# Kernel optimization log

Measured on AMD Instinct MI355X. Metric: run time of the kernel, lower is better.

The kernel has to match this reference:

```python
import jax, jax.numpy as jnp
import numpy as np

B = 4096          # walker batch
S0, S1 = 8, 8     # up / down spins
N = S0 + S1       # total electrons
M = 4             # nucleons
D = 16            # determinants
N_ONE = [256, 256, 256, 256]
N_TWO = [32, 32, 32, 32]


def setup_inputs() -> dict:
    key = jax.random.key(0)
    ks = jax.random.split(key, 16)
    f0 = 8 + 3 * 4 * M              # 56, first-layer one-stream input
    f1 = 3 * N_ONE[0] + 2 * N_TWO[0]  # 832, later-layer one-stream input
    s = 0.05
    return {
        "x": jax.random.normal(ks[0], (B, N, 3), jnp.float32),
        "nucleon_pos": jnp.asarray([[0.0, 0.0, 0.0], [0.0, 0.0, 1.4],
                                    [1.2, 0.0, 0.0], [0.0, 1.2, 0.7]], jnp.float32),
        "v0_w": s * jax.random.normal(ks[1], (N_ONE[0], f0), jnp.float32),
        "v0_b": s * jax.random.normal(ks[2], (N_ONE[0],), jnp.float32),
        "v_w": s * jax.random.normal(ks[3], (3, N_ONE[0], f1), jnp.float32),
        "v_b": s * jax.random.normal(ks[4], (3, N_ONE[0]), jnp.float32),
        "w0_w": s * jax.random.normal(ks[5], (N_TWO[0], 4), jnp.float32),
        "w0_b": s * jax.random.normal(ks[6], (N_TWO[0],), jnp.float32),
        "w_w": s * jax.random.normal(ks[7], (3, N_TWO[0], N_TWO[0]), jnp.float32),
        "w_b": s * jax.random.normal(ks[8], (3, N_TWO[0]), jnp.float32),
        "env_w": s * jax.random.normal(ks[9], (D, N, N_ONE[-1]), jnp.float32),
        "env_g": jax.random.uniform(ks[10], (D, N), jnp.float32),
        "sigma": jax.random.uniform(ks[11], (D, N, M), jnp.float32),
        "pi": jax.random.uniform(ks[12], (D, N, M), jnp.float32),
    }


def _safe_norm(v, axis):
    # ||v||_2 with a zero (not NaN) gradient at v == 0 (diagonal e-e distances).
    s = jnp.sum(v * v, axis=axis)
    return jnp.sqrt(jnp.where(s == 0, 1.0, s)) * (s > 0)


def reference(x, nucleon_pos, v0_w, v0_b, v_w, v_b, w0_w, w0_b, w_w, w_b,
              env_w, env_g, sigma, pi):
    b = x.shape[0]
    # electron-electron stream: [B,N,N,4], [b,i,j] = x_j - x_i, |x_j - x_i|
    tev = x[:, None, :, :] - x[:, :, None, :]
    two = jnp.concatenate([tev, _safe_norm(tev, -1)[..., None]], axis=-1)
    # electron-nucleus: oev[b,m,n] = x_n - R_m  -> [B,M,N,3]
    oev = x[:, None, :, :] - nucleon_pos[:, None, :]
    oed = jnp.linalg.norm(oev, axis=-1)                     # [B,M,N]
    one = jnp.concatenate([oev, oed[..., None]], axis=-1)   # [B,M,N,4]
    one = jnp.transpose(one, (0, 2, 1, 3)).reshape(b, N, 4 * M)  # [B,N,4M]
    oev_p = jnp.transpose(oev, (0, 2, 1, 3))                # [B,N,M,3]

    for l in range(len(N_ONE)):
        g1u = jnp.mean(one[:, :S0], axis=1)                 # [B,F]
        g1d = jnp.mean(one[:, S0:], axis=1)
        g2u = jnp.mean(two[:, :, :S0, :], axis=2)           # [B,N,F2]
        g2d = jnp.mean(two[:, :, S0:, :], axis=2)
        f = jnp.concatenate([
            one,
            jnp.broadcast_to(g1u[:, None], (b, N, g1u.shape[-1])),
            jnp.broadcast_to(g1d[:, None], (b, N, g1d.shape[-1])),
            g2u, g2d], axis=-1)
        Wv, bv = (v0_w, v0_b) if l == 0 else (v_w[l - 1], v_b[l - 1])
        Ww, bw = (w0_w, w0_b) if l == 0 else (w_w[l - 1], w_b[l - 1])
        new_one = jnp.tanh(jnp.einsum('bnf,of->bno', f, Wv) + bv)
        new_two = jnp.tanh(jnp.einsum('bijf,of->bijo', two, Ww) + bw)
        if l > 0 and N_ONE[l] == N_ONE[l - 1] and N_TWO[l] == N_TWO[l - 1]:
            new_one = new_one + one
            new_two = new_two + two
        one, two = new_one, new_two

    r = jnp.linalg.norm(oev_p, axis=-1)                     # [B,N,M]
    F = N_ONE[-1]

    def block(rows, cols):
        ew = env_w[:, rows]                # [D,ni,F]
        eg = env_g[:, rows]                # [D,ni]
        sg = jnp.abs(sigma[:, rows])       # [D,ni,M]
        pw = pi[:, rows]                   # [D,ni,M]
        h = one[:, cols]                   # [B,nj,F]
        rj = r[:, cols]                    # [B,nj,M]
        # sum_f (w*h + g) = w.h + F*g
        lin = jnp.einsum('kif,bjf->bkij', ew, h) + F * eg[None, :, :, None]
        env = jnp.zeros(lin.shape, lin.dtype)
        for m in range(M):                 # small static loop over nucleons
            env = env + pw[None, :, :, None, m] * jnp.exp(
                -sg[None, :, :, None, m] * rj[:, None, None, :, m])
        return lin * env                   # [B,D,ni,nj]

    psi_up = block(slice(0, S0), slice(0, S0))
    psi_dn = block(slice(0, S1), slice(S0, N))  # original reuses row params k*N+i
    d = jnp.linalg.det(psi_up) * jnp.linalg.det(psi_dn)     # [B,D]
    return jnp.sum(d, axis=1)                               # [B]
```

## Files before the change

### kernel.cpp

```cpp
#include <hip/hip_runtime.h>
#include <cmath>

namespace {

typedef unsigned short u16;
typedef unsigned int u32;
using short8  = __attribute__((ext_vector_type(8))) short;
using float4v = __attribute__((ext_vector_type(4))) float;

constexpr size_t MB_HI  = 0;
constexpr size_t MB_LO  = 638976;
constexpr size_t L0_HI  = 1277952;
constexpr size_t L0_LO  = L0_HI + 16384;
constexpr size_t ENV_HI = L0_LO + 16384;
constexpr size_t ENV_LO = ENV_HI + 32768;

__device__ __forceinline__ u16 f2bf(float f) {
    u32 u = __float_as_uint(f);
    u += 0x7FFFu + ((u >> 16) & 1u);
    return (u16)(u >> 16);
}
__device__ __forceinline__ float bf2f(u16 h) {
    return __uint_as_float(((u32)h) << 16);
}
__device__ __forceinline__ float fast_tanh(float x) {
    float e = __expf(-2.f * fabsf(x));
    float t = (1.f - e) * __builtin_amdgcn_rcpf(1.f + e);
    return copysignf(t, x);
}

__global__ void k_prep_main(const float* __restrict__ vw, u16* __restrict__ hi, u16* __restrict__ lo) {
    int id = blockIdx.x * 256 + threadIdx.x;
    int l = id / 212992, rem = id % 212992;
    int ks = rem >> 13;
    int r2 = rem & 8191;
    int nt = r2 >> 9, lane = (r2 >> 3) & 63, j = r2 & 7;
    int n = nt * 16 + (lane & 15);
    int f = ks * 32 + ((lane >> 4) << 3) + j;
    float w = vw[(size_t)(l * 256 + n) * 832 + f];
    u16 h = f2bf(w);
    hi[id] = h; lo[id] = f2bf(w - bf2f(h));
}
__global__ void k_prep_l0(const float* __restrict__ v0w, u16* __restrict__ hi, u16* __restrict__ lo) {
    int id = blockIdx.x * 256 + threadIdx.x;
    int ks = id >> 13;
    int r2 = id & 8191;
    int nt = r2 >> 9, lane = (r2 >> 3) & 63, j = r2 & 7;
    int n = nt * 16 + (lane & 15);
    int f = ks * 32 + ((lane >> 4) << 3) + j;
    float w = (f < 56) ? v0w[n * 56 + f] : 0.f;
    u16 h = f2bf(w);
    hi[id] = h; lo[id] = f2bf(w - bf2f(h));
}
__global__ void k_prep_env(const float* __restrict__ ew, u16* __restrict__ hi, u16* __restrict__ lo) {
    int id = blockIdx.x * 256 + threadIdx.x;
    int ks = id >> 12;
    int r2 = id & 4095;
    int nt = r2 >> 9, lane = (r2 >> 3) & 63, j = r2 & 7;
    int n = nt * 16 + (lane & 15);
    int f = ks * 32 + ((lane >> 4) << 3) + j;
    float w = ew[(size_t)(((n >> 3) * 16) + (n & 7)) * 256 + f];
    u16 h = f2bf(w);
    hi[id] = h; lo[id] = f2bf(w - bf2f(h));
}

template <bool L0, bool RES, bool LAST>
__device__ __forceinline__ void layer_run(
    int t, float (&two)[32], float (&prev)[4][4],
    u16 (*stateF)[32][16][8], u16 (*g2F)[8][16][8], float (*g1s)[256],
    const u16* __restrict__ Bhi, const u16* __restrict__ Blo,
    const float* __restrict__ bvp,
    const float* __restrict__ wwp, const float* __restrict__ bwp)
{
    const int lane = t & 63, wv = t >> 6, quad = lane >> 4, l16 = lane & 15;
    float4v acc[4];
    #pragma unroll
    for (int q = 0; q < 4; ++q) acc[q] = (float4v){0.f, 0.f, 0.f, 0.f};

    const size_t wb0 = (size_t)(wv * 4) * 512 + (size_t)lane * 8;

    auto mfma_step = [&](int ks, short8 Ah, short8 Al) {
        const u16* bh = Bhi + wb0 + (size_t)ks * 8192;
        const u16* bl = Blo + wb0 + (size_t)ks * 8192;
        #pragma unroll
        for (int q = 0; q < 4; ++q) {
            short8 Wh = *(const short8*)(bh + q * 512);
            short8 Wl = *(const short8*)(bl + q * 512);
            acc[q] = __builtin_amdgcn_mfma_f32_16x16x32_bf16(Ah, Wh, acc[q], 0, 0, 0);
            acc[q] = __builtin_amdgcn_mfma_f32_16x16x32_bf16(Al, Wh, acc[q], 0, 0, 0);
            acc[q] = __builtin_amdgcn_mfma_f32_16x16x32_bf16(Ah, Wl, acc[q], 0, 0, 0);
        }
    };

    if (L0) {
        #pragma unroll
        for (int ks = 0; ks < 2; ++ks) {
            short8 Ah = *(const short8*)&g2F[0][ks * 4 + quad][l16][0];
            short8 Al = *(const short8*)&g2F[1][ks * 4 + quad][l16][0];
            mfma_step(ks, Ah, Al);
        }
    } else {
        #pragma unroll 2
        for (int ks = 0; ks < 8; ++ks) {
            short8 Ah = *(const short8*)&stateF[0][ks * 4 + quad][l16][0];
            short8 Al = *(const short8*)&stateF[1][ks * 4 + quad][l16][0];
            mfma_step(ks, Ah, Al);
        }
        #pragma unroll 2
        for (int ks = 8; ks < 24; ++ks) {
            const int ud = (ks < 16) ? 0 : 1;
            const int c0 = ((ks - 8) & 7) * 32 + quad * 8;
            const float* gp = &g1s[ud][c0];
            short8 Ah, Al;
            #pragma unroll
            for (int j = 0; j < 8; ++j) {
                float f = gp[j];
                u16 h = f2bf(f);
                Ah[j] = (short)h;
                Al[j] = (short)f2bf(f - bf2f(h));
            }
            mfma_step(ks, Ah, Al);
        }
        #pragma unroll
        for (int ks = 24; ks < 26; ++ks) {
            short8 Ah = *(const short8*)&g2F[0][(ks - 24) * 4 + quad][l16][0];
            short8 Al = *(const short8*)&g2F[1][(ks - 24) * 4 + quad][l16][0];
            mfma_step(ks, Ah, Al);
        }
    }
    __syncthreads();

    #pragma unroll
    for (int q = 0; q < 4; ++q) {
        const int n = (wv * 4 + q) * 16 + l16;
        const float bvv = bvp[n];
        #pragma unroll
        for (int r = 0; r < 4; ++r) {
            float v = fast_tanh(acc[q][r] + bvv);
            if (RES) v += prev[q][r];
            prev[q][r] = v;
        }
        if (!LAST) {
            float su = 0.f, sd = 0.f;
            #pragma unroll
            for (int r = 0; r < 4; ++r) { if (quad < 2) su += prev[q][r]; else sd += prev[q][r]; }
            su += __shfl_xor(su, 16); su += __shfl_xor(su, 32);
            sd += __shfl_xor(sd, 16); sd += __shfl_xor(sd, 32);
            if (quad == 0) { g1s[0][n] = su * 0.125f; g1s[1][n] = sd * 0.125f; }
        }
        const int ko = n >> 3, jj = n & 7;
        #pragma unroll
        for (int r = 0; r < 4; ++r) {
            const int m = quad * 4 + r;
            u16 h = f2bf(prev[q][r]);
            stateF[0][ko][m][jj] = h;
            stateF[1][ko][m][jj] = f2bf(prev[q][r] - bf2f(h));
        }
    }

    if (!LAST) {
        constexpr int TIN = L0 ? 4 : 32;
        float nt2[32];
        #pragma unroll 4
        for (int o = 0; o < 32; ++o) {
            float a = bwp[o];
            #pragma unroll
            for (int c = 0; c < TIN; ++c) a += two[c] * wwp[o * TIN + c];
            nt2[o] = fast_tanh(a);
            if (RES) nt2[o] += two[o];
        }
        #pragma unroll
        for (int o = 0; o < 32; ++o) two[o] = nt2[o];
        const int i = t >> 4, ud = (t >> 3) & 1;
        #pragma unroll
        for (int c = 0; c < 32; ++c) {
            float v = two[c];
            v += __shfl_xor(v, 1); v += __shfl_xor(v, 2); v += __shfl_xor(v, 4);
            if ((t & 7) == 0) {
                float mn = v * 0.125f;
                int k = ud * 32 + c;
                u16 h = f2bf(mn);
                g2F[0][k >> 3][i][k & 7] = h;
                g2F[1][k >> 3][i][k & 7] = f2bf(mn - bf2f(h));
            }
        }
    }
    __syncthreads();
}

__global__ __launch_bounds__(256, 4) void ferminet_kernel(
    const float* __restrict__ x,
    const float* __restrict__ nuc,
    const float* __restrict__ v0_b,
    const float* __restrict__ v_b,
    const float* __restrict__ w0_w,
    const float* __restrict__ w0_b,
    const float* __restrict__ w_w,
    const float* __restrict__ w_b,
    const float* __restrict__ env_g,
    const float* __restrict__ sigma,
    const float* __restrict__ pi_,
    const u16* __restrict__ wsB,
    float* __restrict__ out)
{
    __shared__ u16  stateF[2][32][16][8];
    __shared__ u16  g2F[2][8][16][8];
    __shared__ float g1s[2][256];
    __shared__ float xs[48];
    __shared__ float rs[64];
    __shared__ float dets[2][16];
    float* psi = (float*)&stateF[0][0][0][0];

    const int t = threadIdx.x;
    const int b = blockIdx.x;
    const int lane = t & 63, wv = t >> 6, quad = lane >> 4, l16 = lane & 15;

    if (t < 48) xs[t] = x[(size_t)b * 48 + t];
    if (t >= 128 && t < 192) ((u32*)&g2F[0][7][0][0])[t - 128] = 0u;
    if (t >= 192 && t < 256) ((u32*)&g2F[1][7][0][0])[t - 192] = 0u;
    __syncthreads();

    if (t < 64) {
        int n = t >> 2, m = t & 3;
        float ox = xs[n * 3 + 0] - nuc[m * 3 + 0];
        float oy = xs[n * 3 + 1] - nuc[m * 3 + 1];
        float oz = xs[n * 3 + 2] - nuc[m * 3 + 2];
        float d = sqrtf(ox * ox + oy * oy + oz * oz);
        rs[n * 4 + m] = d;
        float v[4] = {ox, oy, oz, d};
        #pragma unroll
        for (int c = 0; c < 4; ++c) {
            int k = m * 4 + c;
            u16 h = f2bf(v[c]);
            g2F[0][k >> 3][n][k & 7] = h;
            g2F[1][k >> 3][n][k & 7] = f2bf(v[c] - bf2f(h));
        }
        #pragma unroll
        for (int c = 0; c < 4; ++c) {
            float s = v[c];
            s += __shfl_xor(s, 4); s += __shfl_xor(s, 8); s += __shfl_xor(s, 16);
            if ((n & 7) == 0) {
                float mn = s * 0.125f;
                int k = 16 + (n >> 3) * 16 + m * 4 + c;
                u16 h = f2bf(mn);
                u16 lo = f2bf(mn - bf2f(h));
                #pragma unroll
                for (int mm = 0; mm < 16; ++mm) {
                    g2F[0][k >> 3][mm][k & 7] = h;
                    g2F[1][k >> 3][mm][k & 7] = lo;
                }
            }
        }
    }
    float two[32];
    {
        int i = t >> 4, j = t & 15;
        float dx = xs[j * 3 + 0] - xs[i * 3 + 0];
        float dy = xs[j * 3 + 1] - xs[i * 3 + 1];
        float dz = xs[j * 3 + 2] - xs[i * 3 + 2];
        float s2 = dx * dx + dy * dy + dz * dz;
        float nr = (s2 > 0.f) ? sqrtf(s2) : 0.f;
        two[0] = dx; two[1] = dy; two[2] = dz; two[3] = nr;
        #pragma unroll
        for (int c = 0; c < 4; ++c) {
            float v = two[c];
            v += __shfl_xor(v, 1); v += __shfl_xor(v, 2); v += __shfl_xor(v, 4);
            if ((t & 7) == 0) {
                float mn = v * 0.125f;
                int k = 48 + ((t >> 3) & 1) * 4 + c;
                u16 h = f2bf(mn);
                g2F[0][k >> 3][i][k & 7] = h;
                g2F[1][k >> 3][i][k & 7] = f2bf(mn - bf2f(h));
            }
        }
    }
    __syncthreads();

    float prev[4][4];
    layer_run<true,  false, false>(t, two, prev, stateF, g2F, g1s,
        wsB + L0_HI, wsB + L0_LO, v0_b, w0_w, w0_b);
    layer_run<false, true,  false>(t, two, prev, stateF, g2F, g1s,
        wsB + MB_HI + 0 * 212992, wsB + MB_LO + 0 * 212992, v_b + 0 * 256, w_w + 0 * 1024, w_b + 0 * 32);
    layer_run<false, true,  false>(t, two, prev, stateF, g2F, g1s,
        wsB + MB_HI + 1 * 212992, wsB + MB_LO + 1 * 212992, v_b + 1 * 256, w_w + 1 * 1024, w_b + 1 * 32);
    layer_run<false, true,  true >(t, two, prev, stateF, g2F, g1s,
        wsB + MB_HI + 2 * 212992, wsB + MB_LO + 2 * 212992, v_b + 2 * 256, w_w + 2 * 1024, w_b + 2 * 32);

    {
        float4v ac2[2];
        ac2[0] = (float4v){0.f, 0.f, 0.f, 0.f};
        ac2[1] = (float4v){0.f, 0.f, 0.f, 0.f};
        const size_t wb0 = (size_t)(wv * 2) * 512 + (size_t)lane * 8;
        const u16* Eh = wsB + ENV_HI;
        const u16* El = wsB + ENV_LO;
        #pragma unroll 2
        for (int ks = 0; ks < 8; ++ks) {
            short8 Ah = *(const short8*)&stateF[0][ks * 4 + quad][l16][0];
            short8 Al = *(const short8*)&stateF[1][ks * 4 + quad][l16][0];
            const u16* bh = Eh + wb0 + (size_t)ks * 4096;
            const u16* bl = El + wb0 + (size_t)ks * 4096;
            #pragma unroll
            for (int q = 0; q < 2; ++q) {
                short8 Wh = *(const short8*)(bh + q * 512);
                short8 Wl = *(const short8*)(bl + q * 512);
                ac2[q] = __builtin_amdgcn_mfma_f32_16x16x32_bf16(Ah, Wh, ac2[q], 0, 0, 0);
                ac2[q] = __builtin_amdgcn_mfma_f32_16x16x32_bf16(Al, Wh, ac2[q], 0, 0, 0);
                ac2[q] = __builtin_amdgcn_mfma_f32_16x16x32_bf16(Ah, Wl, ac2[q], 0, 0, 0);
            }
        }
        float vals[2][4];
        int kk[2], ii[2];
        #pragma unroll
        for (int q = 0; q < 2; ++q) {
            const int n = (wv * 2 + q) * 16 + l16;
            const int k = n >> 3, i = n & 7, kif = k * 16 + i;
            kk[q] = k; ii[q] = i;
            const float lc = 256.f * env_g[kif];
            const float4 pw4 = *(const float4*)&pi_[(size_t)kif * 4];
            const float4 sg4 = *(const float4*)&sigma[(size_t)kif * 4];
            const float sg[4] = {fabsf(sg4.x), fabsf(sg4.y), fabsf(sg4.z), fabsf(sg4.w)};
            const float pw[4] = {pw4.x, pw4.y, pw4.z, pw4.w};
            #pragma unroll
            for (int r = 0; r < 4; ++r) {
                const int je = quad * 4 + r;
                float E = 0.f;
                #pragma unroll
                for (int m = 0; m < 4; ++m) E += pw[m] * __expf(-sg[m] * rs[je * 4 + m]);
                vals[q][r] = (ac2[q][r] + lc) * E;
            }
        }
        __syncthreads();
        #pragma unroll
        for (int q = 0; q < 2; ++q) {
            #pragma unroll
            for (int r = 0; r < 4; ++r) {
                const int je = quad * 4 + r;
                const int s = je >> 3, j = je & 7;
                psi[((s * 16 + kk[q]) * 8 + ii[q]) * 8 + j] = vals[q][r];
            }
        }
    }
    __syncthreads();

    if (t < 32) {
        int s = t >> 4, k = t & 15;
        const float* src = psi + (s * 16 + k) * 64;
        float m[8][8];
        #pragma unroll
        for (int i = 0; i < 8; ++i)
            #pragma unroll
            for (int j = 0; j < 8; ++j) m[i][j] = src[i * 8 + j];
        float det = 1.f;
        #pragma unroll
        for (int c = 0; c < 8; ++c) {
            #pragma unroll
            for (int r = c + 1; r < 8; ++r) {
                if (fabsf(m[r][c]) > fabsf(m[c][c])) {
                    det = -det;
                    #pragma unroll
                    for (int j = 0; j < 8; ++j) {
                        float tmp = m[c][j]; m[c][j] = m[r][j]; m[r][j] = tmp;
                    }
                }
            }
            float piv = m[c][c];
            det *= piv;
            if (piv != 0.f) {
                float inv = 1.f / piv;
                #pragma unroll
                for (int r = c + 1; r < 8; ++r) {
                    float fac = m[r][c] * inv;
                    #pragma unroll
                    for (int j = c; j < 8; ++j) m[r][j] -= fac * m[c][j];
                }
            }
        }
        dets[s][k] = det;
    }
    __syncthreads();

    if (t == 0) {
        float s = 0.f;
        #pragma unroll
        for (int k = 0; k < 16; ++k) s += dets[0][k] * dets[1][k];
        out[b] = s;
    }
}

}

extern "C" void kernel_launch(void* const* d_in, const int* in_sizes, int n_in,
                              void* d_out, int out_size, void* d_ws, size_t ws_size,
                              hipStream_t stream) {
    (void)n_in; (void)out_size; (void)ws_size;
    const float* x    = (const float*)d_in[0];
    const float* nuc  = (const float*)d_in[1];
    const float* v0w  = (const float*)d_in[2];
    const float* v0b  = (const float*)d_in[3];
    const float* vw   = (const float*)d_in[4];
    const float* vb   = (const float*)d_in[5];
    const float* w0w  = (const float*)d_in[6];
    const float* w0b  = (const float*)d_in[7];
    const float* ww   = (const float*)d_in[8];
    const float* wb   = (const float*)d_in[9];
    const float* envw = (const float*)d_in[10];
    const float* envg = (const float*)d_in[11];
    const float* sig  = (const float*)d_in[12];
    const float* pii  = (const float*)d_in[13];
    float* out = (float*)d_out;
    u16* wsB = (u16*)d_ws;

    k_prep_main<<<638976 / 256, 256, 0, stream>>>(vw, wsB + MB_HI, wsB + MB_LO);
    k_prep_l0  <<<16384 / 256, 256, 0, stream>>>(v0w, wsB + L0_HI, wsB + L0_LO);
    k_prep_env <<<32768 / 256, 256, 0, stream>>>(envw, wsB + ENV_HI, wsB + ENV_LO);

    const int B = in_sizes[0] / 48;
    ferminet_kernel<<<B, 256, 0, stream>>>(x, nuc, v0b, vb, w0w, w0b,
                                           ww, wb, envg, sig, pii, wsB, out);
}
```

Before: 602.6 us.

## Move two-electron stream layers onto MFMA with split-bf16 weights in shared memory

Replaces the per-thread scalar FMA loop for the two-electron stream (32x32 per pair, per layer) with bf16 hi/lo split MFMA tiles. The two-stream state now lives in shared memory in fragment layout instead of registers, and its weights are preprocessed by a new prep kernel. The one-stream mean g1 is stored pre-split as bf16 fragments, so the MFMA loop no longer converts it from fp32 each step. Launch bounds drop from 4 to 2 waves per SIMD and LDS use grows, which may cut occupancy, and residuals are now rebuilt from bf16 hi+lo pairs.

```diff
diff --git a/kernel.cpp b/kernel.cpp
--- a/kernel.cpp
+++ b/kernel.cpp
@@ -8,12 +8,14 @@
 using short8  = __attribute__((ext_vector_type(8))) short;
 using float4v = __attribute__((ext_vector_type(4))) float;
 
-constexpr size_t MB_HI  = 0;
-constexpr size_t MB_LO  = 638976;
-constexpr size_t L0_HI  = 1277952;
-constexpr size_t L0_LO  = L0_HI + 16384;
-constexpr size_t ENV_HI = L0_LO + 16384;
-constexpr size_t ENV_LO = ENV_HI + 32768;
+constexpr size_t MB_HI   = 0;
+constexpr size_t MB_LO   = 638976;
+constexpr size_t L0_HI   = 1277952;
+constexpr size_t L0_LO   = L0_HI + 16384;
+constexpr size_t ENV_HI  = L0_LO + 16384;
+constexpr size_t ENV_LO  = ENV_HI + 32768;
+constexpr size_t TWOB_HI = ENV_LO + 32768;
+constexpr size_t TWOB_LO = TWOB_HI + 4096;
 
 __device__ __forceinline__ u16 f2bf(float f) {
     u32 u = __float_as_uint(f);
@@ -63,14 +65,28 @@
     u16 h = f2bf(w);
     hi[id] = h; lo[id] = f2bf(w - bf2f(h));
 }
+__global__ void k_prep_two(const float* __restrict__ w0w, const float* __restrict__ ww,
+                           u16* __restrict__ hi, u16* __restrict__ lo) {
+    int id = blockIdx.x * 256 + threadIdx.x;
+    int l = id >> 10, r = id & 1023;
+    int nt = r >> 9, lane = (r >> 3) & 63, j = r & 7;
+    int n = nt * 16 + (lane & 15);
+    int f = ((lane >> 4) << 3) + j;
+    float w;
+    if (l == 0) w = (f < 4) ? w0w[n * 4 + f] : 0.f;
+    else        w = ww[(size_t)(((l - 1) * 32) + n) * 32 + f];
+    u16 h = f2bf(w);
+    hi[id] = h; lo[id] = f2bf(w - bf2f(h));
+}
 
 template <bool L0, bool RES, bool LAST>
 __device__ __forceinline__ void layer_run(
-    int t, float (&two)[32], float (&prev)[4][4],
-    u16 (*stateF)[32][16][8], u16 (*g2F)[8][16][8], float (*g1s)[256],
+    int t, float (&prev)[4][4],
+    u16 (*stateF)[32][16][8], u16 (*twoF)[16][4][16][8],
+    u16 (*g2F)[8][16][8], u16 (*g1F)[2][8][4][8],
     const u16* __restrict__ Bhi, const u16* __restrict__ Blo,
-    const float* __restrict__ bvp,
-    const float* __restrict__ wwp, const float* __restrict__ bwp)
+    const u16* __restrict__ TBhi, const u16* __restrict__ TBlo,
+    const float* __restrict__ bvp, const float* __restrict__ bwp)
 {
     const int lane = t & 63, wv = t >> 6, quad = lane >> 4, l16 = lane & 15;
     float4v acc[4];
@@ -106,19 +122,12 @@
             short8 Al = *(const short8*)&stateF[1][ks * 4 + quad][l16][0];
             mfma_step(ks, Ah, Al);
         }
-        #pragma unroll 2
+        #pragma unroll 4
         for (int ks = 8; ks < 24; ++ks) {
             const int ud = (ks < 16) ? 0 : 1;
-            const int c0 = ((ks - 8) & 7) * 32 + quad * 8;
-            const float* gp = &g1s[ud][c0];
-            short8 Ah, Al;
-            #pragma unroll
-            for (int j = 0; j < 8; ++j) {
-                float f = gp[j];
-                u16 h = f2bf(f);
-                Ah[j] = (short)h;
-                Al[j] = (short)f2bf(f - bf2f(h));
-            }
+            const int kg = (ks - 8) & 7;
+            short8 Ah = *(const short8*)&g1F[0][ud][kg][quad][0];
+            short8 Al = *(const short8*)&g1F[1][ud][kg][quad][0];
             mfma_step(ks, Ah, Al);
         }
         #pragma unroll
@@ -128,6 +137,32 @@
             mfma_step(ks, Ah, Al);
         }
     }
+
+    float4v tac[4][2];
+    #pragma unroll
+    for (int mt = 0; mt < 4; ++mt)
+        #pragma unroll
+        for (int nt = 0; nt < 2; ++nt) tac[mt][nt] = (float4v){0.f, 0.f, 0.f, 0.f};
+    {
+        short8 TWh[2], TWl[2];
+        #pragma unroll
+        for (int nt = 0; nt < 2; ++nt) {
+            TWh[nt] = *(const short8*)(TBhi + nt * 512 + (size_t)lane * 8);
+            TWl[nt] = *(const short8*)(TBlo + nt * 512 + (size_t)lane * 8);
+        }
+        #pragma unroll
+        for (int mt = 0; mt < 4; ++mt) {
+            const int it = wv * 4 + mt;
+            short8 Ah = *(const short8*)&twoF[0][it][quad][l16][0];
+            short8 Al = *(const short8*)&twoF[1][it][quad][l16][0];
+            #pragma unroll
+            for (int nt = 0; nt < 2; ++nt) {
+                tac[mt][nt] = __builtin_amdgcn_mfma_f32_16x16x32_bf16(Ah, TWh[nt], tac[mt][nt], 0, 0, 0);
+                tac[mt][nt] = __builtin_amdgcn_mfma_f32_16x16x32_bf16(Al, TWh[nt], tac[mt][nt], 0, 0, 0);
+                tac[mt][nt] = __builtin_amdgcn_mfma_f32_16x16x32_bf16(Ah, TWl[nt], tac[mt][nt], 0, 0, 0);
+            }
+        }
+    }
     __syncthreads();
 
     #pragma unroll
@@ -146,7 +181,13 @@
             for (int r = 0; r < 4; ++r) { if (quad < 2) su += prev[q][r]; else sd += prev[q][r]; }
             su += __shfl_xor(su, 16); su += __shfl_xor(su, 32);
             sd += __shfl_xor(sd, 16); sd += __shfl_xor(sd, 32);
-            if (quad == 0) { g1s[0][n] = su * 0.125f; g1s[1][n] = sd * 0.125f; }
+            if (quad == 0) {
+                const int kg = n >> 5, qd = (n >> 3) & 3, jj = n & 7;
+                float mu = su * 0.125f, md = sd * 0.125f;
+                u16 hu = f2bf(mu), hd = f2bf(md);
+                g1F[0][0][kg][qd][jj] = hu; g1F[1][0][kg][qd][jj] = f2bf(mu - bf2f(hu));
+                g1F[0][1][kg][qd][jj] = hd; g1F[1][1][kg][qd][jj] = f2bf(md - bf2f(hd));
+            }
         }
         const int ko = n >> 3, jj = n & 7;
         #pragma unroll
@@ -159,43 +200,64 @@
     }
 
     if (!LAST) {
-        constexpr int TIN = L0 ? 4 : 32;
-        float nt2[32];
-        #pragma unroll 4
-        for (int o = 0; o < 32; ++o) {
-            float a = bwp[o];
-            #pragma unroll
-            for (int c = 0; c < TIN; ++c) a += two[c] * wwp[o * TIN + c];
-            nt2[o] = fast_tanh(a);
-            if (RES) nt2[o] += two[o];
-        }
-        #pragma unroll
-        for (int o = 0; o < 32; ++o) two[o] = nt2[o];
-        const int i = t >> 4, ud = (t >> 3) & 1;
-        #pragma unroll
-        for (int c = 0; c < 32; ++c) {
-            float v = two[c];
-            v += __shfl_xor(v, 1); v += __shfl_xor(v, 2); v += __shfl_xor(v, 4);
-            if ((t & 7) == 0) {
-                float mn = v * 0.125f;
-                int k = ud * 32 + c;
-                u16 h = f2bf(mn);
-                g2F[0][k >> 3][i][k & 7] = h;
-                g2F[1][k >> 3][i][k & 7] = f2bf(mn - bf2f(h));
-            }
-        }
-    }
-    __syncthreads();
-}
-
-__global__ __launch_bounds__(256, 4) void ferminet_kernel(
+        #pragma unroll
+        for (int mt = 0; mt < 4; ++mt) {
+            const int it = wv * 4 + mt;
+            float tv[2][4];
+            #pragma unroll
+            for (int nt = 0; nt < 2; ++nt) {
+                const int c = nt * 16 + l16;
+                const float bwv = bwp[c];
+                #pragma unroll
+                for (int r = 0; r < 4; ++r) {
+                    float v = fast_tanh(tac[mt][nt][r] + bwv);
+                    if (RES) {
+                        const int j = quad * 4 + r;
+                        v += bf2f(twoF[0][it][c >> 3][j][c & 7])
+                           + bf2f(twoF[1][it][c >> 3][j][c & 7]);
+                    }
+                    tv[nt][r] = v;
+                }
+            }
+            #pragma unroll
+            for (int nt = 0; nt < 2; ++nt) {
+                float s = tv[nt][0] + tv[nt][1] + tv[nt][2] + tv[nt][3];
+                float su = (quad < 2) ? s : 0.f;
+                float sd = (quad >= 2) ? s : 0.f;
+                su += __shfl_xor(su, 16); su += __shfl_xor(su, 32);
+                sd += __shfl_xor(sd, 16); sd += __shfl_xor(sd, 32);
+                if (quad == 0) {
+                    const int c = nt * 16 + l16;
+                    float mu = su * 0.125f, md = sd * 0.125f;
+                    u16 hu = f2bf(mu), hd = f2bf(md);
+                    g2F[0][c >> 3][it][c & 7] = hu;
+                    g2F[1][c >> 3][it][c & 7] = f2bf(mu - bf2f(hu));
+                    g2F[0][4 + (c >> 3)][it][c & 7] = hd;
+                    g2F[1][4 + (c >> 3)][it][c & 7] = f2bf(md - bf2f(hd));
+                }
+            }
+            #pragma unroll
+            for (int nt = 0; nt < 2; ++nt) {
+                const int c = nt * 16 + l16;
+                #pragma unroll
+                for (int r = 0; r < 4; ++r) {
+                    const int j = quad * 4 + r;
+                    u16 h = f2bf(tv[nt][r]);
+                    twoF[0][it][c >> 3][j][c & 7] = h;
+                    twoF[1][it][c >> 3][j][c & 7] = f2bf(tv[nt][r] - bf2f(h));
+                }
+            }
+        }
+    }
+    __syncthreads();
+}
+
+__global__ __launch_bounds__(256, 2) void ferminet_kernel(
     const float* __restrict__ x,
     const float* __restrict__ nuc,
     const float* __restrict__ v0_b,
     const float* __restrict__ v_b,
-    const float* __restrict__ w0_w,
     const float* __restrict__ w0_b,
-    const float* __restrict__ w_w,
     const float* __restrict__ w_b,
     const float* __restrict__ env_g,
     const float* __restrict__ sigma,
@@ -204,8 +266,9 @@
     float* __restrict__ out)
 {
     __shared__ u16  stateF[2][32][16][8];
+    __shared__ u16  twoF[2][16][4][16][8];
     __shared__ u16  g2F[2][8][16][8];
-    __shared__ float g1s[2][256];
+    __shared__ u16  g1F[2][2][8][4][8];
     __shared__ float xs[48];
     __shared__ float rs[64];
     __shared__ float dets[2][16];
@@ -252,7 +315,6 @@
             }
         }
     }
-    float two[32];
     {
         int i = t >> 4, j = t & 15;
         float dx = xs[j * 3 + 0] - xs[i * 3 + 0];
@@ -260,10 +322,21 @@
         float dz = xs[j * 3 + 2] - xs[i * 3 + 2];
         float s2 = dx * dx + dy * dy + dz * dz;
         float nr = (s2 > 0.f) ? sqrtf(s2) : 0.f;
-        two[0] = dx; two[1] = dy; two[2] = dz; two[3] = nr;
+        float tv[4] = {dx, dy, dz, nr};
+        short8 z = {0, 0, 0, 0, 0, 0, 0, 0};
+        #pragma unroll
+        for (int p = 0; p < 2; ++p)
+            #pragma unroll
+            for (int ko = 0; ko < 4; ++ko) *(short8*)&twoF[p][i][ko][j][0] = z;
         #pragma unroll
         for (int c = 0; c < 4; ++c) {
-            float v = two[c];
+            u16 h = f2bf(tv[c]);
+            twoF[0][i][0][j][c] = h;
+            twoF[1][i][0][j][c] = f2bf(tv[c] - bf2f(h));
+        }
+        #pragma unroll
+        for (int c = 0; c < 4; ++c) {
+            float v = tv[c];
             v += __shfl_xor(v, 1); v += __shfl_xor(v, 2); v += __shfl_xor(v, 4);
             if ((t & 7) == 0) {
                 float mn = v * 0.125f;
@@ -277,14 +350,17 @@
     __syncthreads();
 
     float prev[4][4];
-    layer_run<true,  false, false>(t, two, prev, stateF, g2F, g1s,
-        wsB + L0_HI, wsB + L0_LO, v0_b, w0_w, w0_b);
-    layer_run<false, true,  false>(t, two, prev, stateF, g2F, g1s,
-        wsB + MB_HI + 0 * 212992, wsB + MB_LO + 0 * 212992, v_b + 0 * 256, w_w + 0 * 1024, w_b + 0 * 32);
-    layer_run<false, true,  false>(t, two, prev, stateF, g2F, g1s,
-        wsB + MB_HI + 1 * 212992, wsB + MB_LO + 1 * 212992, v_b + 1 * 256, w_w + 1 * 1024, w_b + 1 * 32);
-    layer_run<false, true,  true >(t, two, prev, stateF, g2F, g1s,
-        wsB + MB_HI + 2 * 212992, wsB + MB_LO + 2 * 212992, v_b + 2 * 256, w_w + 2 * 1024, w_b + 2 * 32);
+    layer_run<true,  false, false>(t, prev, stateF, twoF, g2F, g1F,
+        wsB + L0_HI, wsB + L0_LO, wsB + TWOB_HI, wsB + TWOB_LO, v0_b, w0_b);
+    layer_run<false, true,  false>(t, prev, stateF, twoF, g2F, g1F,
+        wsB + MB_HI + 0 * 212992, wsB + MB_LO + 0 * 212992,
+        wsB + TWOB_HI + 1024, wsB + TWOB_LO + 1024, v_b + 0 * 256, w_b + 0 * 32);
+    layer_run<false, true,  false>(t, prev, stateF, twoF, g2F, g1F,
+        wsB + MB_HI + 1 * 212992, wsB + MB_LO + 1 * 212992,
+        wsB + TWOB_HI + 2048, wsB + TWOB_LO + 2048, v_b + 1 * 256, w_b + 1 * 32);
+    layer_run<false, true,  true >(t, prev, stateF, twoF, g2F, g1F,
+        wsB + MB_HI + 2 * 212992, wsB + MB_LO + 2 * 212992,
+        wsB + TWOB_HI + 3072, wsB + TWOB_LO + 3072, v_b + 2 * 256, w_b + 2 * 32);
 
     {
         float4v ac2[2];
@@ -413,8 +489,9 @@
     k_prep_main<<<638976 / 256, 256, 0, stream>>>(vw, wsB + MB_HI, wsB + MB_LO);
     k_prep_l0  <<<16384 / 256, 256, 0, stream>>>(v0w, wsB + L0_HI, wsB + L0_LO);
     k_prep_env <<<32768 / 256, 256, 0, stream>>>(envw, wsB + ENV_HI, wsB + ENV_LO);
+    k_prep_two <<<4096 / 256, 256, 0, stream>>>(w0w, ww, wsB + TWOB_HI, wsB + TWOB_LO);
 
     const int B = in_sizes[0] / 48;
-    ferminet_kernel<<<B, 256, 0, stream>>>(x, nuc, v0b, vb, w0w, w0b,
-                                           ww, wb, envg, sig, pii, wsB, out);
-}
+    ferminet_kernel<<<B, 256, 0, stream>>>(x, nuc, v0b, vb, w0b, wb,
+                                           envg, sig, pii, wsB, out);
+}
```

New measurement: 569.6 us. 1.06x faster.
